# Kernel tuning notes

Measured on AMD Instinct MI355X. Metric: run time of the kernel, lower is better.

The kernel has to match this reference:

```python
import jax, jax.numpy as jnp
import numpy as np

B, S, E, H, D = 4, 2048, 1024, 16, 64


def setup_inputs() -> dict:
    key = jax.random.key(0)
    ks = jax.random.split(key, 10)
    s_in = 1.0 / np.sqrt(E)
    s_out = 1.0 / np.sqrt(H * D)
    return {
        "x": jax.random.normal(ks[0], (B, S, E), dtype=jnp.float32),
        "wq": jax.random.uniform(ks[1], (H, E, D), jnp.float32, -s_in, s_in),
        "bq": jax.random.uniform(ks[2], (H, D), jnp.float32, -s_in, s_in),
        "wk": jax.random.uniform(ks[3], (H, E, D), jnp.float32, -s_in, s_in),
        "bk": jax.random.uniform(ks[4], (H, D), jnp.float32, -s_in, s_in),
        "wv": jax.random.uniform(ks[5], (H, E, D), jnp.float32, -s_in, s_in),
        "bv": jax.random.uniform(ks[6], (H, D), jnp.float32, -s_in, s_in),
        "wo": jax.random.uniform(ks[7], (H * D, E), jnp.float32, -s_out, s_out),
        "bo": jax.random.uniform(ks[8], (E,), jnp.float32, -s_out, s_out),
    }


def reference(x, wq, bq, wk, bk, wv, bv, wo, bo):
    # Batched equivalent of the per-head Python loop: project all heads at once.
    q = jnp.einsum("bse,hed->bhsd", x, wq) + bq[None, :, None, :]
    k = jnp.einsum("bse,hed->bhsd", x, wk) + bk[None, :, None, :]
    v = jnp.einsum("bse,hed->bhsd", x, wv) + bv[None, :, None, :]
    scale = 1.0 / jnp.sqrt(jnp.asarray(D, dtype=x.dtype))
    scores = jnp.einsum("bhsd,bhtd->bhst", q, k) * scale  # [B,H,S,S]
    causal = jnp.tril(jnp.ones((S, S), dtype=bool))
    scores = jnp.where(causal[None, None], scores, jnp.asarray(-jnp.inf, x.dtype))
    p = jax.nn.softmax(scores, axis=-1)
    o = jnp.einsum("bhst,bhtd->bhsd", p, v)
    # concat heads along last dim (head order matches the torch cat order)
    o = jnp.transpose(o, (0, 2, 1, 3)).reshape(B, S, H * D)
    y = o @ wo + bo  # output projection; dropout is identity in eval
    return y
```

## Files before the change

kernel.cpp:

```cpp
#include <hip/hip_runtime.h>
#include <math.h>

#define B_ 4
#define S_ 2048
#define E_ 1024
#define H_ 16
#define D_ 64

using f32x4 = __attribute__((ext_vector_type(4))) float;
using s16x8 = __attribute__((ext_vector_type(8))) short;

__device__ __forceinline__ unsigned short f2bf(float f) {
    unsigned int u = __float_as_uint(f);
    u = (u + 0x7FFFu + ((u >> 16) & 1u)) >> 16;
    return (unsigned short)u;
}

__device__ __forceinline__ unsigned int cvt_pk_bf16(float lo, float hi) {
    unsigned int r;
    asm("v_cvt_pk_bf16_f32 %0, %1, %2" : "=v"(r) : "v"(lo), "v"(hi));
    return r;
}

__device__ __forceinline__ float fast_exp2(float x) {
#if __has_builtin(__builtin_amdgcn_exp2f)
    return __builtin_amdgcn_exp2f(x);
#else
    return exp2f(x);
#endif
}

__device__ __forceinline__ void load_lds16(const void* g, void* l) {
    __builtin_amdgcn_global_load_lds(
        (const __attribute__((address_space(1))) void*)g,
        (__attribute__((address_space(3))) void*)l, 16, 0, 0);
}

#define WAITV(n) asm volatile("s_waitcnt vmcnt(" #n ")" ::: "memory")

#define QSCALE 0.18033688011112042f

__global__ __launch_bounds__(256)
void cast_x(const float* __restrict__ in, unsigned short* __restrict__ out)
{
    const size_t idx = (size_t)blockIdx.x * 2048 + threadIdx.x * 8;
    const float4 v0 = *(const float4*)&in[idx];
    const float4 v1 = *(const float4*)&in[idx + 4];
    uint4 p;
    p.x = (unsigned)f2bf(v0.x) | ((unsigned)f2bf(v0.y) << 16);
    p.y = (unsigned)f2bf(v0.z) | ((unsigned)f2bf(v0.w) << 16);
    p.z = (unsigned)f2bf(v1.x) | ((unsigned)f2bf(v1.y) << 16);
    p.w = (unsigned)f2bf(v1.z) | ((unsigned)f2bf(v1.w) << 16);
    *(uint4*)&out[idx] = p;
}

__global__ __launch_bounds__(256)
void transpose_w(const float* __restrict__ wq, const float* __restrict__ wk,
                 const float* __restrict__ wv, const float* __restrict__ wo,
                 unsigned short* __restrict__ Wqkvt, unsigned short* __restrict__ Wot)
{
    __shared__ float T[64][68];
    const int z = blockIdx.z;
    const float* in;
    unsigned short* out;
    int inStride, r0, c0;
    if (z < 48) {
        if (blockIdx.y != 0) return;
        const int t = z >> 4, h = z & 15;
        const float* W = (t == 0) ? wq : ((t == 1) ? wk : wv);
        in = W + (size_t)h * (E_ * D_);
        inStride = 64;
        out = Wqkvt + (size_t)(t * 1024 + h * 64) * 1024;
        r0 = blockIdx.x * 64; c0 = 0;
    } else {
        in = wo; inStride = 1024;
        out = Wot;
        r0 = blockIdx.x * 64; c0 = blockIdx.y * 64;
    }
    const int tid = threadIdx.x;
    #pragma unroll
    for (int i = 0; i < 4; ++i) {
        const int e = tid + i * 256;
        const int row = e >> 4, c4 = e & 15;
        const float4 v = *(const float4*)&in[(size_t)(r0 + row) * inStride + c0 + c4 * 4];
        T[row][c4 * 4 + 0] = v.x; T[row][c4 * 4 + 1] = v.y;
        T[row][c4 * 4 + 2] = v.z; T[row][c4 * 4 + 3] = v.w;
    }
    __syncthreads();
    #pragma unroll
    for (int i = 0; i < 2; ++i) {
        const int e = tid + i * 256;
        const int c = e >> 3, ch = e & 7;
        unsigned short h8[8];
        #pragma unroll
        for (int j = 0; j < 8; ++j) h8[j] = f2bf(T[ch * 8 + j][c]);
        uint4 p;
        p.x = (unsigned)h8[0] | ((unsigned)h8[1] << 16);
        p.y = (unsigned)h8[2] | ((unsigned)h8[3] << 16);
        p.z = (unsigned)h8[4] | ((unsigned)h8[5] << 16);
        p.w = (unsigned)h8[6] | ((unsigned)h8[7] << 16);
        *(uint4*)&out[(size_t)(c0 + c) * 1024 + r0 + ch * 8] = p;
    }
}

template<int MODE>
__global__ __launch_bounds__(512, 2)
void gemm_mfma(const unsigned short* __restrict__ A,
               const unsigned short* __restrict__ Bt,
               const float* __restrict__ bq, const float* __restrict__ bk,
               const float* __restrict__ bv, const float* __restrict__ bo,
               unsigned short* __restrict__ Qb, unsigned short* __restrict__ Kb,
               unsigned short* __restrict__ Vt, float* __restrict__ Cout)
{
    __shared__ short As[3][128 * 64];
    __shared__ short Bs[3][256 * 64];

    const int tid  = threadIdx.x;
    const int w    = tid >> 6, lane = tid & 63;
    const int g    = lane >> 4, l15 = lane & 15;
    const int wm   = w >> 2, wn = w & 3;
    const int mbase = blockIdx.x * 128;
    const int nbase = blockIdx.y * 256;

    const int srow   = lane >> 3;
    const int schunk = (lane & 7) ^ srow;
    const size_t aoff = (size_t)(mbase + srow) * 1024 + schunk * 8;
    const size_t boff = (size_t)(nbase + srow) * 1024 + schunk * 8;

    f32x4 acc[4][4];
    #pragma unroll
    for (int mt = 0; mt < 4; ++mt)
        #pragma unroll
        for (int nt = 0; nt < 4; ++nt)
            acc[mt][nt] = (f32x4){0.f, 0.f, 0.f, 0.f};

    auto STAGE_A = [&](int t, int buf, int i) {
        const int u = w * 2 + i;
        load_lds16(&A[aoff + (size_t)(u * 8) * 1024 + t * 64], &As[buf][u * 512]);
    };
    auto STAGE_B = [&](int t, int buf, int i) {
        const int u = w * 4 + i;
        load_lds16(&Bt[boff + (size_t)(u * 8) * 1024 + t * 64], &Bs[buf][u * 512]);
    };

    STAGE_A(0, 0, 0); STAGE_A(0, 0, 1);
    STAGE_B(0, 0, 0); STAGE_B(0, 0, 1); STAGE_B(0, 0, 2); STAGE_B(0, 0, 3);
    STAGE_A(1, 1, 0); STAGE_A(1, 1, 1);
    STAGE_B(1, 1, 0); STAGE_B(1, 1, 1); STAGE_B(1, 1, 2); STAGE_B(1, 1, 3);

    const int pr = l15 & 7;

    #pragma unroll 1
    for (int t = 0; t < 16; ++t) {
        const int buf = t % 3;
        const int nb  = (t + 2) % 3;
        if (t < 15) { WAITV(6); } else { WAITV(0); }
        __builtin_amdgcn_s_barrier();
        __builtin_amdgcn_sched_barrier(0);

        s16x8 af[4], bf[4];

        {
            const int pc = (g ^ pr) * 8;
            #pragma unroll
            for (int mt = 0; mt < 4; ++mt)
                af[mt] = *(const s16x8*)&As[buf][(wm * 64 + mt * 16 + l15) * 64 + pc];
            #pragma unroll
            for (int nt = 0; nt < 4; ++nt)
                bf[nt] = *(const s16x8*)&Bs[buf][(wn * 64 + nt * 16 + l15) * 64 + pc];
        }
        if (t + 2 < 16) { STAGE_A(t + 2, nb, 0); STAGE_A(t + 2, nb, 1); STAGE_B(t + 2, nb, 0); }
        __builtin_amdgcn_s_barrier();
        __builtin_amdgcn_sched_barrier(0);
        __builtin_amdgcn_s_setprio(1);
        #pragma unroll
        for (int mt = 0; mt < 4; ++mt)
            #pragma unroll
            for (int nt = 0; nt < 4; ++nt)
                acc[mt][nt] = __builtin_amdgcn_mfma_f32_16x16x32_bf16(
                    af[mt], bf[nt], acc[mt][nt], 0, 0, 0);
        __builtin_amdgcn_s_setprio(0);
        __builtin_amdgcn_s_barrier();

        {
            const int pc = ((4 + g) ^ pr) * 8;
            #pragma unroll
            for (int mt = 0; mt < 4; ++mt)
                af[mt] = *(const s16x8*)&As[buf][(wm * 64 + mt * 16 + l15) * 64 + pc];
            #pragma unroll
            for (int nt = 0; nt < 4; ++nt)
                bf[nt] = *(const s16x8*)&Bs[buf][(wn * 64 + nt * 16 + l15) * 64 + pc];
        }
        if (t + 2 < 16) { STAGE_B(t + 2, nb, 1); STAGE_B(t + 2, nb, 2); STAGE_B(t + 2, nb, 3); }
        __builtin_amdgcn_s_barrier();
        __builtin_amdgcn_sched_barrier(0);
        __builtin_amdgcn_s_setprio(1);
        #pragma unroll
        for (int mt = 0; mt < 4; ++mt)
            #pragma unroll
            for (int nt = 0; nt < 4; ++nt)
                acc[mt][nt] = __builtin_amdgcn_mfma_f32_16x16x32_bf16(
                    af[mt], bf[nt], acc[mt][nt], 0, 0, 0);
        __builtin_amdgcn_s_setprio(0);
    }

    #pragma unroll
    for (int nt = 0; nt < 4; ++nt) {
        const int ncol = nbase + wn * 64 + nt * 16 + l15;
        if (MODE == 0) {
            const int tt = ncol >> 10;
            const int hh = (ncol >> 6) & 15;
            const int d  = ncol & 63;
            const float* bias = (tt == 0) ? bq : ((tt == 1) ? bk : bv);
            const float sc = (tt == 0) ? QSCALE : 1.0f;
            const float bval = bias[hh * 64 + d];
            #pragma unroll
            for (int mt = 0; mt < 4; ++mt)
                #pragma unroll
                for (int r = 0; r < 4; ++r) {
                    const int m = mbase + wm * 64 + mt * 16 + g * 4 + r;
                    const int b = m >> 11, s = m & 2047;
                    const unsigned short val = f2bf((acc[mt][nt][r] + bval) * sc);
                    if (tt == 2)
                        Vt[((size_t)(b * 16 + hh) * 64 + d) * 2048 + s] = val;
                    else {
                        unsigned short* Out = (tt == 0) ? Qb : Kb;
                        Out[((size_t)(b * 16 + hh) * 2048 + s) * 64 + d] = val;
                    }
                }
        } else {
            const float bval = bo[ncol];
            #pragma unroll
            for (int mt = 0; mt < 4; ++mt)
                #pragma unroll
                for (int r = 0; r < 4; ++r) {
                    const int m = mbase + wm * 64 + mt * 16 + g * 4 + r;
                    Cout[(size_t)m * 1024 + ncol] = acc[mt][nt][r] + bval;
                }
        }
    }
}

#define LDK 72
__global__ __launch_bounds__(512, 2)
void attn_mfma(const unsigned short* __restrict__ Qb,
               const unsigned short* __restrict__ Kb,
               const unsigned short* __restrict__ Vt,
               unsigned short* __restrict__ O)
{
    __shared__ short Kls[2][64 * LDK];
    __shared__ short Vls[2][64 * LDK];
    __shared__ short Pls[8][16 * LDK];

    const int tid  = threadIdx.x;
    const int w    = tid >> 6;
    const int lane = tid & 63;
    const int g    = lane >> 4;
    const int l15  = lane & 15;
    const int j    = blockIdx.x;
    const int j2   = 15 - j;
    const int h    = blockIdx.y;
    const int b    = blockIdx.z;

    const size_t hb = (size_t)(b * 16 + h) * (2048 * 64);
    const int qH = j2 * 128 + w * 16;
    const int qL = j * 128 + w * 16;

    s16x8 aqH[2], aqL[2];
    {
        const int rh = qH + l15, rl = qL + l15;
        aqH[0] = *(const s16x8*)&Qb[hb + (size_t)rh * 64 + g * 8];
        aqH[1] = *(const s16x8*)&Qb[hb + (size_t)rh * 64 + 32 + g * 8];
        aqL[0] = *(const s16x8*)&Qb[hb + (size_t)rl * 64 + g * 8];
        aqL[1] = *(const s16x8*)&Qb[hb + (size_t)rl * 64 + 32 + g * 8];
    }

    const s16x8 ones = (s16x8){(short)0x3F80, (short)0x3F80, (short)0x3F80,
                               (short)0x3F80, (short)0x3F80, (short)0x3F80,
                               (short)0x3F80, (short)0x3F80};

    f32x4 lsumHa = (f32x4){0.f,0.f,0.f,0.f};
    f32x4 lsumLa = (f32x4){0.f,0.f,0.f,0.f};
    f32x4 OH[4], OL[4];
    #pragma unroll
    for (int nt = 0; nt < 4; ++nt) { OH[nt] = (f32x4){0.f,0.f,0.f,0.f}; OL[nt] = (f32x4){0.f,0.f,0.f,0.f}; }

    const int stages      = 32 - 2 * j;
    const int lightStages = 2 * j + 2;

    const int srow = tid >> 3, spart = tid & 7;
    uint4 kreg = *(const uint4*)&Kb[hb + (size_t)srow * 64 + spart * 8];
    uint4 vreg = *(const uint4*)&Vt[hb + (size_t)srow * 2048 + spart * 8];

    for (int t = 0; t < stages; ++t) {
        const int t0  = t * 64;
        const int buf = t & 1;
        *(uint4*)&Kls[buf][srow * LDK + spart * 8] = kreg;
        *(uint4*)&Vls[buf][srow * LDK + spart * 8] = vreg;
        if (t + 1 < stages) {
            kreg = *(const uint4*)&Kb[hb + (size_t)(t0 + 64 + srow) * 64 + spart * 8];
            vreg = *(const uint4*)&Vt[hb + (size_t)srow * 2048 + t0 + 64 + spart * 8];
        }
        __syncthreads();

        #pragma unroll
        for (int half = 0; half < 2; ++half) {
            if (half == 1 && t >= lightStages) break;
            const s16x8* aq   = (half == 0) ? aqH : aqL;
            const int qbase   = (half == 0) ? qH : qL;
            f32x4* Oacc       = (half == 0) ? OH : OL;
            f32x4* lsa        = (half == 0) ? &lsumHa : &lsumLa;

            f32x4 Sf[4];
            #pragma unroll
            for (int ct = 0; ct < 4; ++ct) {
                f32x4 acc = (f32x4){0.f, 0.f, 0.f, 0.f};
                const s16x8 bk0 = *(const s16x8*)&Kls[buf][(ct * 16 + l15) * LDK + g * 8];
                const s16x8 bk1 = *(const s16x8*)&Kls[buf][(ct * 16 + l15) * LDK + 32 + g * 8];
                acc = __builtin_amdgcn_mfma_f32_16x16x32_bf16(bk0, aq[0], acc, 0, 0, 0);
                acc = __builtin_amdgcn_mfma_f32_16x16x32_bf16(bk1, aq[1], acc, 0, 0, 0);
                Sf[ct] = acc;
            }

            if (t0 + 63 > qbase) {
                const int query = qbase + l15;
                #pragma unroll
                for (int ct = 0; ct < 4; ++ct) {
                    const int kbase = t0 + ct * 16 + g * 4;
                    #pragma unroll
                    for (int r = 0; r < 4; ++r)
                        if (kbase + r > query) Sf[ct][r] = -1e30f;
                }
            }

            #pragma unroll
            for (int ct = 0; ct < 4; ++ct)
                #pragma unroll
                for (int r = 0; r < 4; ++r) Sf[ct][r] = fast_exp2(Sf[ct][r]);

            #pragma unroll
            for (int ct = 0; ct < 4; ++ct) {
                uint2 pw;
                pw.x = cvt_pk_bf16(Sf[ct][0], Sf[ct][1]);
                pw.y = cvt_pk_bf16(Sf[ct][2], Sf[ct][3]);
                *(uint2*)&Pls[w][l15 * LDK + ct * 16 + g * 4] = pw;
            }

            const s16x8 pf0 = *(const s16x8*)&Pls[w][l15 * LDK + g * 8];
            const s16x8 pf1 = *(const s16x8*)&Pls[w][l15 * LDK + 32 + g * 8];
            *lsa = __builtin_amdgcn_mfma_f32_16x16x32_bf16(ones, pf0, *lsa, 0, 0, 0);
            *lsa = __builtin_amdgcn_mfma_f32_16x16x32_bf16(ones, pf1, *lsa, 0, 0, 0);
            #pragma unroll
            for (int nt = 0; nt < 4; ++nt) {
                const s16x8 bv0 = *(const s16x8*)&Vls[buf][(nt * 16 + l15) * LDK + g * 8];
                const s16x8 bv1 = *(const s16x8*)&Vls[buf][(nt * 16 + l15) * LDK + 32 + g * 8];
                Oacc[nt] = __builtin_amdgcn_mfma_f32_16x16x32_bf16(bv0, pf0, Oacc[nt], 0, 0, 0);
                Oacc[nt] = __builtin_amdgcn_mfma_f32_16x16x32_bf16(bv1, pf1, Oacc[nt], 0, 0, 0);
            }
        }
    }

    const float invH = 1.0f / lsumHa[0];
    const float invL = 1.0f / lsumLa[0];

    #pragma unroll
    for (int half = 0; half < 2; ++half) {
        const f32x4* Oacc = (half == 0) ? OH : OL;
        const float  inv  = (half == 0) ? invH : invL;
        const int query   = ((half == 0) ? qH : qL) + l15;
        #pragma unroll
        for (int nt = 0; nt < 4; ++nt) {
            uint2 pk;
            pk.x = cvt_pk_bf16(Oacc[nt][0] * inv, Oacc[nt][1] * inv);
            pk.y = cvt_pk_bf16(Oacc[nt][2] * inv, Oacc[nt][3] * inv);
            *(uint2*)&O[(size_t)(b * 2048 + query) * 1024 + h * 64 + nt * 16 + g * 4] = pk;
        }
    }
}

extern "C" void kernel_launch(void* const* d_in, const int* in_sizes, int n_in,
                              void* d_out, int out_size, void* d_ws, size_t ws_size,
                              hipStream_t stream) {
    const float* x  = (const float*)d_in[0];
    const float* wq = (const float*)d_in[1];
    const float* bq = (const float*)d_in[2];
    const float* wk = (const float*)d_in[3];
    const float* bk = (const float*)d_in[4];
    const float* wv = (const float*)d_in[5];
    const float* bv = (const float*)d_in[6];
    const float* wo = (const float*)d_in[7];
    const float* bo = (const float*)d_in[8];
    float* out = (float*)d_out;

    const size_t hsz = (size_t)B_ * H_ * S_ * D_;
    unsigned short* xb    = (unsigned short*)d_ws;
    unsigned short* Wqkvt = xb + hsz;
    unsigned short* Wot   = Wqkvt + (size_t)3072 * 1024;
    unsigned short* Qb    = Wot + (size_t)1024 * 1024;
    unsigned short* Kb    = Qb + hsz;
    unsigned short* Vt    = Kb + hsz;
    unsigned short* Ob    = Vt + hsz;

    cast_x<<<4096, 256, 0, stream>>>(x, xb);
    transpose_w<<<dim3(16, 16, 49), 256, 0, stream>>>(wq, wk, wv, wo, Wqkvt, Wot);
    gemm_mfma<0><<<dim3(64, 12), 512, 0, stream>>>(
        xb, Wqkvt, bq, bk, bv, nullptr, Qb, Kb, Vt, nullptr);
    attn_mfma<<<dim3(8, H_, B_), 512, 0, stream>>>(Qb, Kb, Vt, Ob);
    gemm_mfma<1><<<dim3(64, 4), 512, 0, stream>>>(
        Ob, Wot, nullptr, nullptr, nullptr, bo, nullptr, nullptr, nullptr, out);
}
```

Baseline: 264.9 us.

## Software-pipeline LDS fragment loads with MFMA using double-buffered register fragments

Restructures the GEMM main loop so the second half-tile fragments and the next tile's first-half fragments are read from LDS while MFMAs on already-loaded fragments run. It uses two register fragment sets and lgkmcnt waits instead of the four barriers per iteration. All global-to-LDS staging for tile t+2 is now issued at once. This aims to hide LDS read latency and cut barrier stalls, at the cost of more VGPRs, which may reduce occupancy. It also relies on the ordering of the manual waitcnt for correctness with the 3-stage ring buffer.

```diff
diff --git a/kernel.cpp b/kernel.cpp
--- a/kernel.cpp
+++ b/kernel.cpp
@@ -37,6 +37,8 @@
 }
 
 #define WAITV(n) asm volatile("s_waitcnt vmcnt(" #n ")" ::: "memory")
+#define WAITL(n) asm volatile("s_waitcnt lgkmcnt(" #n ")" ::: "memory")
+#define SCHEDB __builtin_amdgcn_sched_barrier(0)
 
 #define QSCALE 0.18033688011112042f
 
@@ -134,44 +136,33 @@
         for (int nt = 0; nt < 4; ++nt)
             acc[mt][nt] = (f32x4){0.f, 0.f, 0.f, 0.f};
 
-    auto STAGE_A = [&](int t, int buf, int i) {
-        const int u = w * 2 + i;
-        load_lds16(&A[aoff + (size_t)(u * 8) * 1024 + t * 64], &As[buf][u * 512]);
+    auto STAGE = [&](int t, int buf) {
+        #pragma unroll
+        for (int i = 0; i < 2; ++i) {
+            const int u = w * 2 + i;
+            load_lds16(&A[aoff + (size_t)(u * 8) * 1024 + t * 64], &As[buf][u * 512]);
+        }
+        #pragma unroll
+        for (int i = 0; i < 4; ++i) {
+            const int u = w * 4 + i;
+            load_lds16(&Bt[boff + (size_t)(u * 8) * 1024 + t * 64], &Bs[buf][u * 512]);
+        }
     };
-    auto STAGE_B = [&](int t, int buf, int i) {
-        const int u = w * 4 + i;
-        load_lds16(&Bt[boff + (size_t)(u * 8) * 1024 + t * 64], &Bs[buf][u * 512]);
+
+    const int pr  = l15 & 7;
+    const int pc0 = (g ^ pr) * 8;
+    const int pc1 = ((4 + g) ^ pr) * 8;
+
+    s16x8 a0[4], b0[4], a1[4], b1[4];
+    auto LDF = [&](s16x8* af, s16x8* bf, int buf, int pc) {
+        #pragma unroll
+        for (int mt = 0; mt < 4; ++mt)
+            af[mt] = *(const s16x8*)&As[buf][(wm * 64 + mt * 16 + l15) * 64 + pc];
+        #pragma unroll
+        for (int nt = 0; nt < 4; ++nt)
+            bf[nt] = *(const s16x8*)&Bs[buf][(wn * 64 + nt * 16 + l15) * 64 + pc];
     };
-
-    STAGE_A(0, 0, 0); STAGE_A(0, 0, 1);
-    STAGE_B(0, 0, 0); STAGE_B(0, 0, 1); STAGE_B(0, 0, 2); STAGE_B(0, 0, 3);
-    STAGE_A(1, 1, 0); STAGE_A(1, 1, 1);
-    STAGE_B(1, 1, 0); STAGE_B(1, 1, 1); STAGE_B(1, 1, 2); STAGE_B(1, 1, 3);
-
-    const int pr = l15 & 7;
-
-    #pragma unroll 1
-    for (int t = 0; t < 16; ++t) {
-        const int buf = t % 3;
-        const int nb  = (t + 2) % 3;
-        if (t < 15) { WAITV(6); } else { WAITV(0); }
-        __builtin_amdgcn_s_barrier();
-        __builtin_amdgcn_sched_barrier(0);
-
-        s16x8 af[4], bf[4];
-
-        {
-            const int pc = (g ^ pr) * 8;
-            #pragma unroll
-            for (int mt = 0; mt < 4; ++mt)
-                af[mt] = *(const s16x8*)&As[buf][(wm * 64 + mt * 16 + l15) * 64 + pc];
-            #pragma unroll
-            for (int nt = 0; nt < 4; ++nt)
-                bf[nt] = *(const s16x8*)&Bs[buf][(wn * 64 + nt * 16 + l15) * 64 + pc];
-        }
-        if (t + 2 < 16) { STAGE_A(t + 2, nb, 0); STAGE_A(t + 2, nb, 1); STAGE_B(t + 2, nb, 0); }
-        __builtin_amdgcn_s_barrier();
-        __builtin_amdgcn_sched_barrier(0);
+    auto MFMA16 = [&](const s16x8* af, const s16x8* bf) {
         __builtin_amdgcn_s_setprio(1);
         #pragma unroll
         for (int mt = 0; mt < 4; ++mt)
@@ -180,28 +171,28 @@
                 acc[mt][nt] = __builtin_amdgcn_mfma_f32_16x16x32_bf16(
                     af[mt], bf[nt], acc[mt][nt], 0, 0, 0);
         __builtin_amdgcn_s_setprio(0);
-        __builtin_amdgcn_s_barrier();
-
-        {
-            const int pc = ((4 + g) ^ pr) * 8;
-            #pragma unroll
-            for (int mt = 0; mt < 4; ++mt)
-                af[mt] = *(const s16x8*)&As[buf][(wm * 64 + mt * 16 + l15) * 64 + pc];
-            #pragma unroll
-            for (int nt = 0; nt < 4; ++nt)
-                bf[nt] = *(const s16x8*)&Bs[buf][(wn * 64 + nt * 16 + l15) * 64 + pc];
-        }
-        if (t + 2 < 16) { STAGE_B(t + 2, nb, 1); STAGE_B(t + 2, nb, 2); STAGE_B(t + 2, nb, 3); }
-        __builtin_amdgcn_s_barrier();
-        __builtin_amdgcn_sched_barrier(0);
-        __builtin_amdgcn_s_setprio(1);
-        #pragma unroll
-        for (int mt = 0; mt < 4; ++mt)
-            #pragma unroll
-            for (int nt = 0; nt < 4; ++nt)
-                acc[mt][nt] = __builtin_amdgcn_mfma_f32_16x16x32_bf16(
-                    af[mt], bf[nt], acc[mt][nt], 0, 0, 0);
-        __builtin_amdgcn_s_setprio(0);
+    };
+
+    STAGE(0, 0); STAGE(1, 1);
+    WAITV(6);
+    __builtin_amdgcn_s_barrier();
+    LDF(a0, b0, 0, pc0);
+
+    #pragma unroll 1
+    for (int t = 0; t < 16; ++t) {
+        const int buf = t % 3;
+        LDF(a1, b1, buf, pc1);
+        if (t + 2 < 16) STAGE(t + 2, (t + 2) % 3);
+        WAITL(8); SCHEDB;
+        MFMA16(a0, b0);
+        WAITL(0); SCHEDB;
+        if (t < 15) {
+            if (t < 14) { WAITV(6); } else { WAITV(0); }
+            __builtin_amdgcn_s_barrier();
+            LDF(a0, b0, (t + 1) % 3, pc0);
+            WAITL(8); SCHEDB;
+        }
+        MFMA16(a1, b1);
     }
 
     #pragma unroll
```

Measured after the change: 258.7 us. -2.4%, faster.
